# Performance work log

Measured on AMD Instinct MI355X. Metric: run time of the kernel, lower is better.

## Reference

```python
import jax, jax.numpy as jnp
import numpy as np

B = 32           # batch
LATENT = 512     # latent_dim
U = 256          # lstm_units
T = 2048


def setup_inputs() -> dict:
    key = jax.random.key(0)
    ks = jax.random.split(key, 8)
    s = lambda k, shape: jax.random.normal(k, shape, jnp.float32) * 0.05
    return {
        "context_vector": jax.random.normal(ks[0], (B, LATENT), jnp.float32),
        # context_dense: Dense(latent_dim -> lstm_units, relu)
        "Wc": s(ks[1], (LATENT, U)), "bc": jnp.zeros((U,), jnp.float32),
        # lstm1: input dim 2 (coords), keras gate order i,f,g,o in 4*U kernel
        "K1": s(ks[2], (2, 4 * U)), "R1": s(ks[3], (U, 4 * U)), "b1": jnp.zeros((4 * U,), jnp.float32),
        # lstm2: input dim U
        "K2": s(ks[4], (U, 4 * U)), "R2": s(ks[5], (U, 4 * U)), "b2": jnp.zeros((4 * U,), jnp.float32),
        # output_dense: Dense(lstm_units -> 2, sigmoid)
        "Wo": s(ks[6], (U, 2)), "bo": jnp.zeros((2,), jnp.float32),
    }


def _lstm_cell(x, h, c, K, R, b):
    # Keras LSTM cell: gates ordered [i, f, g, o]; sigmoid recurrent activation, tanh activation.
    z = x @ K + h @ R + b                      # [B, 4U]
    i, f, g, o = jnp.split(z, 4, axis=-1)
    c_new = jax.nn.sigmoid(f) * c + jax.nn.sigmoid(i) * jnp.tanh(g)
    h_new = jax.nn.sigmoid(o) * jnp.tanh(c_new)
    return h_new, c_new


def reference(context_vector, Wc, bc, K1, R1, b1, K2, R2, b2, Wo, bo):
    # initial states: h1 = relu(Dense(context)), c1 = h2 = c2 = 0
    h1 = jax.nn.relu(context_vector @ Wc + bc)           # [B, U]
    c1 = jnp.zeros_like(h1)
    h2 = jnp.zeros_like(h1)
    c2 = jnp.zeros_like(h1)
    start = jnp.full((context_vector.shape[0], 2), 0.5, context_vector.dtype)  # start token

    def step(carry, _):
        inp, h1, c1, h2, c2 = carry
        h1, c1 = _lstm_cell(inp, h1, c1, K1, R1, b1)
        h2, c2 = _lstm_cell(h1, h2, c2, K2, R2, b2)
        out = jax.nn.sigmoid(h2 @ Wo + bo)               # [B, 2]
        return (out, h1, c1, h2, c2), out

    _, ys = jax.lax.scan(step, (start, h1, c1, h2, c2), None, length=T)
    return jnp.transpose(ys, (1, 0, 2))                  # [B, T, 2]
```

## Files before the change

### kernel.cpp

```cpp
#include <hip/hip_runtime.h>


#define TSTEPS 2048
#define UNITS  256
#define NB     32
#define NSL    64
#define NTHR   512

typedef float f4 __attribute__((ext_vector_type(4)));

constexpr int CH   = 72;
constexpr int VECF = 4 * CH;
constexpr int BUFW = 4 * VECF;
constexpr int SMEM_BYTES = 84 * 1024;
constexpr int RECF = 8;

__device__ __forceinline__ float sigm(float x) { return 1.f / (1.f + expf(-x)); }

__device__ __forceinline__ float mk_chk(float a, float b, float c, float d, float t) {
  return __fadd_rn(__fadd_rn(__fadd_rn(__fadd_rn(a, b), c), d), t);
}

__device__ __forceinline__ void load_rec(const float* p, f4& a, float& chk) {
  asm volatile("global_load_dwordx4 %0, %2, off sc0 sc1\n\t"
               "global_load_dword %1, %2, off offset:16 sc0 sc1\n\t"
               "s_waitcnt vmcnt(0)"
               : "=&v"(a), "=&v"(chk) : "v"(p) : "memory");
}
__device__ __forceinline__ void store_rec(float* p, const f4& d, float chk) {
  asm volatile("global_store_dwordx4 %0, %1, off sc0 sc1\n\t"
               "global_store_dword %0, %2, off offset:16 sc0 sc1"
               :: "v"(p), "v"(d), "v"(chk) : "memory");
}

__device__ __forceinline__ bool poll2(const float* p0, const float* p1, float tag,
                                      f4& d0, f4& d1, bool ok) {
  if (!ok) return false;
  bool v0 = false, v1 = false;
  int it = 0;
  for (;;) {
    if (!v0) {
      f4 a; float cc; load_rec(p0, a, cc);
      if (__float_as_uint(cc) == __float_as_uint(mk_chk(a.x, a.y, a.z, a.w, tag))) { d0 = a; v0 = true; }
    }
    if (!v1) {
      f4 a; float cc; load_rec(p1, a, cc);
      if (__float_as_uint(cc) == __float_as_uint(mk_chk(a.x, a.y, a.z, a.w, tag))) { d1 = a; v1 = true; }
    }
    if (__all(v0 && v1)) return true;
    if (++it > (1 << 18)) return false;
    if (it > 16) __builtin_amdgcn_s_sleep(1);
  }
}

__device__ __forceinline__ void publish(float* ring, int k, int b, int slice,
                                        int lane, float hn) {
  const float h0 = __shfl(hn, 0), h1 = __shfl(hn, 1),
              h2 = __shfl(hn, 2), h3 = __shfl(hn, 3);
  const float chk = mk_chk(h0, h1, h2, h3, (float)k);
  if (lane == 0) {
    f4 d; d.x = h0; d.y = h1; d.z = h2; d.w = h3;
    store_rec(ring + (((k & 1) * NB + b) * NSL + slice) * RECF, d, chk);
  }
}

__device__ __forceinline__ const float* recp(const float* ring, int k, int b, int sl) {
  return ring + (((k & 1) * NB + b) * NSL + sl) * RECF;
}

__global__ __launch_bounds__(NTHR) void swd_kernel(
    const float* __restrict__ ctx, const float* __restrict__ Wc, const float* __restrict__ bc,
    const float* __restrict__ K1, const float* __restrict__ R1, const float* __restrict__ b1,
    const float* __restrict__ K2, const float* __restrict__ R2, const float* __restrict__ b2,
    const float* __restrict__ Wo, const float* __restrict__ bo,
    float* __restrict__ dout, float* __restrict__ ring1, float* __restrict__ ring2)
{
  extern __shared__ float sm[];
  const int wgid  = blockIdx.x;
  const int layer = wgid >> 7;
  const int half  = (wgid >> 6) & 1;
  const int slice = wgid & 63;
  const int tid = threadIdx.x, lane = tid & 63, wid = tid >> 6;
  const int c = lane & 15, kk = lane >> 4, q = c >> 2, u = c & 3;
  const int gc = q * UNITS + slice * 4 + u;
  const int b0 = half * 16 + wid * 2, b1v = b0 + 1;
  float* buf = sm + wid * BUFW;
  bool ok = true;

  if (layer == 0) {
    float w1[64];
    #pragma unroll
    for (int j = 0; j < 64; ++j) w1[j] = R1[(64 * kk + j) * 1024 + gc];
    const float k1a = K1[gc], k1b = K1[1024 + gc], bb1 = b1[gc];
    float wo0[4], wo1[4];
    #pragma unroll
    for (int m = 0; m < 4; ++m) {
      wo0[m] = Wo[(4 * lane + m) * 2];
      wo1[m] = Wo[(4 * lane + m) * 2 + 1];
    }
    const float bo0 = bo[0], bo1 = bo[1];

    #pragma unroll
    for (int bi = 0; bi < 2; ++bi) {
      const int b = b0 + bi;
      float hv[4];
      #pragma unroll
      for (int uu = 0; uu < 4; ++uu) {
        float p = 0.f;
        const float* cb = ctx + b * 512;
        const float* wc = Wc + slice * 4 + uu;
        #pragma unroll
        for (int m = 0; m < 8; ++m) p = fmaf(cb[lane * 8 + m], wc[(lane * 8 + m) * UNITS], p);
        #pragma unroll
        for (int d = 32; d; d >>= 1) p += __shfl_down(p, d);
        hv[uu] = fmaxf(p + bc[slice * 4 + uu], 0.f);
      }
      const float chk = mk_chk(hv[0], hv[1], hv[2], hv[3], 0.f);
      if (lane == 0) {
        f4 d; d.x = hv[0]; d.y = hv[1]; d.z = hv[2]; d.w = hv[3];
        store_rec(ring1 + ((0 * NB + b) * NSL + slice) * RECF, d, chk);
      }
    }

    float c1a = 0.f, c1b = 0.f;
    float* bufA0 = buf;
    float* bufA1 = buf + VECF;
    for (int s = 0; s < TSTEPS; ++s) {
      f4 d0, d1;
      ok = poll2(recp(ring1, s, b0, lane), recp(ring1, s, b1v, lane), (float)s, d0, d1, ok);
      *(f4*)(bufA0 + kk * CH + 4 * c) = d0;
      *(f4*)(bufA1 + kk * CH + 4 * c) = d1;
      float ax0 = 0.f, ay0 = 0.f, az0 = 0.f, aw0 = 0.f;
      float ax1 = 0.f, ay1 = 0.f, az1 = 0.f, aw1 = 0.f;
      #pragma unroll
      for (int j = 0; j < 16; ++j) {
        const f4 h0 = *(const f4*)(bufA0 + kk * CH + 4 * j);
        const f4 h1 = *(const f4*)(bufA1 + kk * CH + 4 * j);
        ax0 = fmaf(w1[4 * j + 0], h0.x, ax0); ay0 = fmaf(w1[4 * j + 1], h0.y, ay0);
        az0 = fmaf(w1[4 * j + 2], h0.z, az0); aw0 = fmaf(w1[4 * j + 3], h0.w, aw0);
        ax1 = fmaf(w1[4 * j + 0], h1.x, ax1); ay1 = fmaf(w1[4 * j + 1], h1.y, ay1);
        az1 = fmaf(w1[4 * j + 2], h1.z, az1); aw1 = fmaf(w1[4 * j + 3], h1.w, aw1);
      }
      float part0 = (ax0 + ay0) + (az0 + aw0);
      float part1 = (ax1 + ay1) + (az1 + aw1);
      part0 += __shfl_down(part0, 16); part0 += __shfl_down(part0, 32);
      part1 += __shfl_down(part1, 16); part1 += __shfl_down(part1, 32);
      float x00 = 0.5f, x01 = 0.5f, x10 = 0.5f, x11 = 0.5f;
      if (s > 0) {
        f4 g0, g1;
        ok = poll2(recp(ring2, s, b0, lane), recp(ring2, s, b1v, lane), (float)s, g0, g1, ok);
        float po00 = g0.x * wo0[0] + g0.y * wo0[1] + g0.z * wo0[2] + g0.w * wo0[3];
        float po01 = g0.x * wo1[0] + g0.y * wo1[1] + g0.z * wo1[2] + g0.w * wo1[3];
        float po10 = g1.x * wo0[0] + g1.y * wo0[1] + g1.z * wo0[2] + g1.w * wo0[3];
        float po11 = g1.x * wo1[0] + g1.y * wo1[1] + g1.z * wo1[2] + g1.w * wo1[3];
        #pragma unroll
        for (int d = 1; d < 64; d <<= 1) {
          po00 += __shfl_xor(po00, d); po01 += __shfl_xor(po01, d);
          po10 += __shfl_xor(po10, d); po11 += __shfl_xor(po11, d);
        }
        x00 = sigm(po00 + bo0); x01 = sigm(po01 + bo1);
        x10 = sigm(po10 + bo0); x11 = sigm(po11 + bo1);
        if (slice == 0 && lane == 0) {
          *(float2*)(dout + (b0  * TSTEPS + s - 1) * 2) = make_float2(x00, x01);
          *(float2*)(dout + (b1v * TSTEPS + s - 1) * 2) = make_float2(x10, x11);
        }
      }
      {
        const float z = part0 + x00 * k1a + x01 * k1b + bb1;
        const float act = (q == 2) ? tanhf(z) : sigm(z);
        const float gi = __shfl(act, u),     gf = __shfl(act, 4 + u),
                    gg = __shfl(act, 8 + u), go = __shfl(act, 12 + u);
        const float cn = gf * c1a + gi * gg;
        const float hn = go * tanhf(cn);
        c1a = cn;
        publish(ring1, s + 1, b0, slice, lane, hn);
      }
      {
        const float z = part1 + x10 * k1a + x11 * k1b + bb1;
        const float act = (q == 2) ? tanhf(z) : sigm(z);
        const float gi = __shfl(act, u),     gf = __shfl(act, 4 + u),
                    gg = __shfl(act, 8 + u), go = __shfl(act, 12 + u);
        const float cn = gf * c1b + gi * gg;
        const float hn = go * tanhf(cn);
        c1b = cn;
        publish(ring1, s + 1, b1v, slice, lane, hn);
      }
    }
    if (slice == 0) {
      f4 g0, g1;
      ok = poll2(recp(ring2, TSTEPS, b0, lane), recp(ring2, TSTEPS, b1v, lane),
                 (float)TSTEPS, g0, g1, ok);
      float po00 = g0.x * wo0[0] + g0.y * wo0[1] + g0.z * wo0[2] + g0.w * wo0[3];
      float po01 = g0.x * wo1[0] + g0.y * wo1[1] + g0.z * wo1[2] + g0.w * wo1[3];
      float po10 = g1.x * wo0[0] + g1.y * wo0[1] + g1.z * wo0[2] + g1.w * wo0[3];
      float po11 = g1.x * wo1[0] + g1.y * wo1[1] + g1.z * wo1[2] + g1.w * wo1[3];
      #pragma unroll
      for (int d = 1; d < 64; d <<= 1) {
        po00 += __shfl_xor(po00, d); po01 += __shfl_xor(po01, d);
        po10 += __shfl_xor(po10, d); po11 += __shfl_xor(po11, d);
      }
      if (lane == 0) {
        *(float2*)(dout + (b0  * TSTEPS + TSTEPS - 1) * 2) =
            make_float2(sigm(po00 + bo0), sigm(po01 + bo1));
        *(float2*)(dout + (b1v * TSTEPS + TSTEPS - 1) * 2) =
            make_float2(sigm(po10 + bo0), sigm(po11 + bo1));
      }
    }
  } else {
    float wk[64], wr[64];
    #pragma unroll
    for (int j = 0; j < 64; ++j) {
      wk[j] = K2[(64 * kk + j) * 1024 + gc];
      wr[j] = R2[(64 * kk + j) * 1024 + gc];
    }
    const float bb2 = b2[gc];
    float c2a = 0.f, c2b = 0.f;
    float* bh20 = buf;
    float* bh21 = buf + VECF;
    float* bh10 = buf + 2 * VECF;
    float* bh11 = buf + 3 * VECF;
    for (int s = 0; s < TSTEPS; ++s) {
      f4 g0 = {0.f, 0.f, 0.f, 0.f}, g1 = {0.f, 0.f, 0.f, 0.f};
      if (s > 0)
        ok = poll2(recp(ring2, s, b0, lane), recp(ring2, s, b1v, lane), (float)s, g0, g1, ok);
      *(f4*)(bh20 + kk * CH + 4 * c) = g0;
      *(f4*)(bh21 + kk * CH + 4 * c) = g1;
      float rx0 = 0.f, ry0 = 0.f, rz0 = 0.f, rw0 = 0.f;
      float rx1 = 0.f, ry1 = 0.f, rz1 = 0.f, rw1 = 0.f;
      #pragma unroll
      for (int j = 0; j < 16; ++j) {
        const f4 h0 = *(const f4*)(bh20 + kk * CH + 4 * j);
        const f4 h1 = *(const f4*)(bh21 + kk * CH + 4 * j);
        rx0 = fmaf(wr[4 * j + 0], h0.x, rx0); ry0 = fmaf(wr[4 * j + 1], h0.y, ry0);
        rz0 = fmaf(wr[4 * j + 2], h0.z, rz0); rw0 = fmaf(wr[4 * j + 3], h0.w, rw0);
        rx1 = fmaf(wr[4 * j + 0], h1.x, rx1); ry1 = fmaf(wr[4 * j + 1], h1.y, ry1);
        rz1 = fmaf(wr[4 * j + 2], h1.z, rz1); rw1 = fmaf(wr[4 * j + 3], h1.w, rw1);
      }
      f4 d0, d1;
      ok = poll2(recp(ring1, s + 1, b0, lane), recp(ring1, s + 1, b1v, lane),
                 (float)(s + 1), d0, d1, ok);
      *(f4*)(bh10 + kk * CH + 4 * c) = d0;
      *(f4*)(bh11 + kk * CH + 4 * c) = d1;
      float kx0 = 0.f, ky0 = 0.f, kz0 = 0.f, kw0 = 0.f;
      float kx1 = 0.f, ky1 = 0.f, kz1 = 0.f, kw1 = 0.f;
      #pragma unroll
      for (int j = 0; j < 16; ++j) {
        const f4 h0 = *(const f4*)(bh10 + kk * CH + 4 * j);
        const f4 h1 = *(const f4*)(bh11 + kk * CH + 4 * j);
        kx0 = fmaf(wk[4 * j + 0], h0.x, kx0); ky0 = fmaf(wk[4 * j + 1], h0.y, ky0);
        kz0 = fmaf(wk[4 * j + 2], h0.z, kz0); kw0 = fmaf(wk[4 * j + 3], h0.w, kw0);
        kx1 = fmaf(wk[4 * j + 0], h1.x, kx1); ky1 = fmaf(wk[4 * j + 1], h1.y, ky1);
        kz1 = fmaf(wk[4 * j + 2], h1.z, kz1); kw1 = fmaf(wk[4 * j + 3], h1.w, kw1);
      }
      float part0 = ((rx0 + ry0) + (rz0 + rw0)) + ((kx0 + ky0) + (kz0 + kw0));
      float part1 = ((rx1 + ry1) + (rz1 + rw1)) + ((kx1 + ky1) + (kz1 + kw1));
      part0 += __shfl_down(part0, 16); part0 += __shfl_down(part0, 32);
      part1 += __shfl_down(part1, 16); part1 += __shfl_down(part1, 32);
      {
        const float z = part0 + bb2;
        const float act = (q == 2) ? tanhf(z) : sigm(z);
        const float gi = __shfl(act, u),     gf = __shfl(act, 4 + u),
                    gg = __shfl(act, 8 + u), go = __shfl(act, 12 + u);
        const float cn = gf * c2a + gi * gg;
        const float hn = go * tanhf(cn);
        c2a = cn;
        publish(ring2, s + 1, b0, slice, lane, hn);
      }
      {
        const float z = part1 + bb2;
        const float act = (q == 2) ? tanhf(z) : sigm(z);
        const float gi = __shfl(act, u),     gf = __shfl(act, 4 + u),
                    gg = __shfl(act, 8 + u), go = __shfl(act, 12 + u);
        const float cn = gf * c2b + gi * gg;
        const float hn = go * tanhf(cn);
        c2b = cn;
        publish(ring2, s + 1, b1v, slice, lane, hn);
      }
    }
  }
  (void)ok;
}

extern "C" void kernel_launch(void* const* d_in, const int* in_sizes, int n_in,
                              void* d_out, int out_size, void* d_ws, size_t ws_size,
                              hipStream_t stream) {
  (void)in_sizes; (void)n_in; (void)out_size; (void)ws_size;
  const float* ctx = (const float*)d_in[0];
  const float* Wc  = (const float*)d_in[1];
  const float* bc  = (const float*)d_in[2];
  const float* K1  = (const float*)d_in[3];
  const float* R1  = (const float*)d_in[4];
  const float* b1  = (const float*)d_in[5];
  const float* K2  = (const float*)d_in[6];
  const float* R2  = (const float*)d_in[7];
  const float* b2  = (const float*)d_in[8];
  const float* Wo  = (const float*)d_in[9];
  const float* bo  = (const float*)d_in[10];

  float* ring1 = (float*)d_ws;
  float* ring2 = ring1 + 2 * NB * NSL * RECF;

  hipFuncSetAttribute((const void*)swd_kernel,
                      hipFuncAttributeMaxDynamicSharedMemorySize, SMEM_BYTES);
  swd_kernel<<<dim3(256), dim3(NTHR), SMEM_BYTES, stream>>>(
      ctx, Wc, bc, K1, R1, b1, K2, R2, b2, Wo, bo,
      (float*)d_out, ring1, ring2);
}
```

Before: 30.75 ms.

## Issue paired ring polls together, skip self-slice poll, batch output writes

The polling routine now issues both batch-row record loads before one wait instead of two serialized load-wait pairs. Each block keeps its own freshly published slice locally instead of re-reading it from global memory. The poll for the next step moves to the end of the iteration, right after publishing. The writer block buffers sigmoid outputs in shared memory and flushes them as vector stores every 32 steps instead of issuing per-step scalar stores. This shortens the latency of the inter-block handoff on the serial recurrence, at the cost of more restructured control flow and a shorter timeout bound.

```diff
diff --git a/kernel.cpp b/kernel.cpp
--- a/kernel.cpp
+++ b/kernel.cpp
@@ -12,6 +12,7 @@
 constexpr int CH   = 72;
 constexpr int VECF = 4 * CH;
 constexpr int BUFW = 4 * VECF;
+constexpr int HIST_OFF = 8 * BUFW;
 constexpr int SMEM_BYTES = 84 * 1024;
 constexpr int RECF = 8;
 
@@ -21,51 +22,51 @@
   return __fadd_rn(__fadd_rn(__fadd_rn(__fadd_rn(a, b), c), d), t);
 }
 
-__device__ __forceinline__ void load_rec(const float* p, f4& a, float& chk) {
-  asm volatile("global_load_dwordx4 %0, %2, off sc0 sc1\n\t"
-               "global_load_dword %1, %2, off offset:16 sc0 sc1\n\t"
-               "s_waitcnt vmcnt(0)"
-               : "=&v"(a), "=&v"(chk) : "v"(p) : "memory");
-}
 __device__ __forceinline__ void store_rec(float* p, const f4& d, float chk) {
   asm volatile("global_store_dwordx4 %0, %1, off sc0 sc1\n\t"
                "global_store_dword %0, %2, off offset:16 sc0 sc1"
                :: "v"(p), "v"(d), "v"(chk) : "memory");
 }
 
-__device__ __forceinline__ bool poll2(const float* p0, const float* p1, float tag,
-                                      f4& d0, f4& d1, bool ok) {
+__device__ __forceinline__ void load2_rec(const float* p0, const float* p1,
+                                          f4& a0, float& c0, f4& a1, float& c1) {
+  asm volatile("global_load_dwordx4 %0, %4, off sc0 sc1\n\t"
+               "global_load_dword %1, %4, off offset:16 sc0 sc1\n\t"
+               "global_load_dwordx4 %2, %5, off sc0 sc1\n\t"
+               "global_load_dword %3, %5, off offset:16 sc0 sc1\n\t"
+               "s_waitcnt vmcnt(0)"
+               : "=&v"(a0), "=&v"(c0), "=&v"(a1), "=&v"(c1)
+               : "v"(p0), "v"(p1) : "memory");
+}
+
+__device__ __forceinline__ const float* recp(const float* ring, int k, int b, int sl) {
+  return ring + (((k & 1) * NB + b) * NSL + sl) * RECF;
+}
+
+__device__ __forceinline__ bool pollj(const float* p0, const float* p1, float tag,
+                                      f4& d0, f4& d1, bool v0, bool v1, bool ok) {
   if (!ok) return false;
-  bool v0 = false, v1 = false;
   int it = 0;
-  for (;;) {
-    if (!v0) {
-      f4 a; float cc; load_rec(p0, a, cc);
-      if (__float_as_uint(cc) == __float_as_uint(mk_chk(a.x, a.y, a.z, a.w, tag))) { d0 = a; v0 = true; }
-    }
-    if (!v1) {
-      f4 a; float cc; load_rec(p1, a, cc);
-      if (__float_as_uint(cc) == __float_as_uint(mk_chk(a.x, a.y, a.z, a.w, tag))) { d1 = a; v1 = true; }
-    }
-    if (__all(v0 && v1)) return true;
-    if (++it > (1 << 18)) return false;
-    if (it > 16) __builtin_amdgcn_s_sleep(1);
+  while (!__all(v0 && v1)) {
+    f4 a0, a1; float c0, c1;
+    load2_rec(p0, p1, a0, c0, a1, c1);
+    if (!v0 && __float_as_uint(c0) == __float_as_uint(mk_chk(a0.x, a0.y, a0.z, a0.w, tag))) { d0 = a0; v0 = true; }
+    if (!v1 && __float_as_uint(c1) == __float_as_uint(mk_chk(a1.x, a1.y, a1.z, a1.w, tag))) { d1 = a1; v1 = true; }
+    if (++it > (1 << 15)) return false;
+    if (it > 64) __builtin_amdgcn_s_sleep(1);
   }
-}
-
-__device__ __forceinline__ void publish(float* ring, int k, int b, int slice,
-                                        int lane, float hn) {
+  return true;
+}
+
+__device__ __forceinline__ f4 publish(float* ring, int k, int b, int slice,
+                                      int lane, float hn) {
   const float h0 = __shfl(hn, 0), h1 = __shfl(hn, 1),
               h2 = __shfl(hn, 2), h3 = __shfl(hn, 3);
-  const float chk = mk_chk(h0, h1, h2, h3, (float)k);
-  if (lane == 0) {
-    f4 d; d.x = h0; d.y = h1; d.z = h2; d.w = h3;
-    store_rec(ring + (((k & 1) * NB + b) * NSL + slice) * RECF, d, chk);
-  }
-}
-
-__device__ __forceinline__ const float* recp(const float* ring, int k, int b, int sl) {
-  return ring + (((k & 1) * NB + b) * NSL + sl) * RECF;
+  f4 d; d.x = h0; d.y = h1; d.z = h2; d.w = h3;
+  if (lane == 0)
+    store_rec(ring + (((k & 1) * NB + b) * NSL + slice) * RECF, d,
+              mk_chk(h0, h1, h2, h3, (float)k));
+  return d;
 }
 
 __global__ __launch_bounds__(NTHR) void swd_kernel(
@@ -99,11 +100,14 @@
       wo1[m] = Wo[(4 * lane + m) * 2 + 1];
     }
     const float bo0 = bo[0], bo1 = bo[1];
-
+    const bool writer = (slice == 0);
+    float* hist = sm + HIST_OFF + wid * 128;
+
+    f4 self0, self1;
     #pragma unroll
     for (int bi = 0; bi < 2; ++bi) {
       const int b = b0 + bi;
-      float hv[4];
+      float hn = 0.f;
       #pragma unroll
       for (int uu = 0; uu < 4; ++uu) {
         float p = 0.f;
@@ -113,29 +117,29 @@
         for (int m = 0; m < 8; ++m) p = fmaf(cb[lane * 8 + m], wc[(lane * 8 + m) * UNITS], p);
         #pragma unroll
         for (int d = 32; d; d >>= 1) p += __shfl_down(p, d);
-        hv[uu] = fmaxf(p + bc[slice * 4 + uu], 0.f);
-      }
-      const float chk = mk_chk(hv[0], hv[1], hv[2], hv[3], 0.f);
-      if (lane == 0) {
-        f4 d; d.x = hv[0]; d.y = hv[1]; d.z = hv[2]; d.w = hv[3];
-        store_rec(ring1 + ((0 * NB + b) * NSL + slice) * RECF, d, chk);
-      }
+        const float r = __shfl(p, 0);
+        if (lane == uu) hn = fmaxf(r + bc[slice * 4 + uu], 0.f);
+      }
+      const f4 sf = publish(ring1, 0, b, slice, lane, hn);
+      if (bi == 0) self0 = sf; else self1 = sf;
+    }
+    {
+      f4 d0, d1; const bool v = (lane == slice);
+      if (v) { d0 = self0; d1 = self1; }
+      ok = pollj(recp(ring1, 0, b0, lane), recp(ring1, 0, b1v, lane), 0.f, d0, d1, v, v, ok);
+      *(f4*)(buf + kk * CH + 4 * c) = d0;
+      *(f4*)(buf + VECF + kk * CH + 4 * c) = d1;
+      asm volatile("" ::: "memory");
     }
 
     float c1a = 0.f, c1b = 0.f;
-    float* bufA0 = buf;
-    float* bufA1 = buf + VECF;
     for (int s = 0; s < TSTEPS; ++s) {
-      f4 d0, d1;
-      ok = poll2(recp(ring1, s, b0, lane), recp(ring1, s, b1v, lane), (float)s, d0, d1, ok);
-      *(f4*)(bufA0 + kk * CH + 4 * c) = d0;
-      *(f4*)(bufA1 + kk * CH + 4 * c) = d1;
       float ax0 = 0.f, ay0 = 0.f, az0 = 0.f, aw0 = 0.f;
       float ax1 = 0.f, ay1 = 0.f, az1 = 0.f, aw1 = 0.f;
       #pragma unroll
       for (int j = 0; j < 16; ++j) {
-        const f4 h0 = *(const f4*)(bufA0 + kk * CH + 4 * j);
-        const f4 h1 = *(const f4*)(bufA1 + kk * CH + 4 * j);
+        const f4 h0 = *(const f4*)(buf + kk * CH + 4 * j);
+        const f4 h1 = *(const f4*)(buf + VECF + kk * CH + 4 * j);
         ax0 = fmaf(w1[4 * j + 0], h0.x, ax0); ay0 = fmaf(w1[4 * j + 1], h0.y, ay0);
         az0 = fmaf(w1[4 * j + 2], h0.z, az0); aw0 = fmaf(w1[4 * j + 3], h0.w, aw0);
         ax1 = fmaf(w1[4 * j + 0], h1.x, ax1); ay1 = fmaf(w1[4 * j + 1], h1.y, ay1);
@@ -145,10 +149,12 @@
       float part1 = (ax1 + ay1) + (az1 + aw1);
       part0 += __shfl_down(part0, 16); part0 += __shfl_down(part0, 32);
       part1 += __shfl_down(part1, 16); part1 += __shfl_down(part1, 32);
+
       float x00 = 0.5f, x01 = 0.5f, x10 = 0.5f, x11 = 0.5f;
       if (s > 0) {
         f4 g0, g1;
-        ok = poll2(recp(ring2, s, b0, lane), recp(ring2, s, b1v, lane), (float)s, g0, g1, ok);
+        ok = pollj(recp(ring2, s, b0, lane), recp(ring2, s, b1v, lane), (float)s,
+                   g0, g1, false, false, ok);
         float po00 = g0.x * wo0[0] + g0.y * wo0[1] + g0.z * wo0[2] + g0.w * wo0[3];
         float po01 = g0.x * wo1[0] + g0.y * wo1[1] + g0.z * wo1[2] + g0.w * wo1[3];
         float po10 = g1.x * wo0[0] + g1.y * wo0[1] + g1.z * wo0[2] + g1.w * wo0[3];
@@ -160,36 +166,57 @@
         }
         x00 = sigm(po00 + bo0); x01 = sigm(po01 + bo1);
         x10 = sigm(po10 + bo0); x11 = sigm(po11 + bo1);
-        if (slice == 0 && lane == 0) {
-          *(float2*)(dout + (b0  * TSTEPS + s - 1) * 2) = make_float2(x00, x01);
-          *(float2*)(dout + (b1v * TSTEPS + s - 1) * 2) = make_float2(x10, x11);
+        if (writer && lane == 0) {
+          *(float2*)(hist + ((s - 1) & 31) * 2)      = make_float2(x00, x01);
+          *(float2*)(hist + 64 + ((s - 1) & 31) * 2) = make_float2(x10, x11);
         }
       }
-      {
-        const float z = part0 + x00 * k1a + x01 * k1b + bb1;
+
+      {
+        const float z   = part0 + x00 * k1a + x01 * k1b + bb1;
         const float act = (q == 2) ? tanhf(z) : sigm(z);
         const float gi = __shfl(act, u),     gf = __shfl(act, 4 + u),
                     gg = __shfl(act, 8 + u), go = __shfl(act, 12 + u);
         const float cn = gf * c1a + gi * gg;
-        const float hn = go * tanhf(cn);
         c1a = cn;
-        publish(ring1, s + 1, b0, slice, lane, hn);
-      }
-      {
-        const float z = part1 + x10 * k1a + x11 * k1b + bb1;
+        self0 = publish(ring1, s + 1, b0, slice, lane, go * tanhf(cn));
+      }
+      {
+        const float z   = part1 + x10 * k1a + x11 * k1b + bb1;
         const float act = (q == 2) ? tanhf(z) : sigm(z);
         const float gi = __shfl(act, u),     gf = __shfl(act, 4 + u),
                     gg = __shfl(act, 8 + u), go = __shfl(act, 12 + u);
         const float cn = gf * c1b + gi * gg;
-        const float hn = go * tanhf(cn);
         c1b = cn;
-        publish(ring1, s + 1, b1v, slice, lane, hn);
-      }
-    }
-    if (slice == 0) {
+        self1 = publish(ring1, s + 1, b1v, slice, lane, go * tanhf(cn));
+      }
+
+      if (writer && s >= 32 && (s & 31) == 0) {
+        asm volatile("" ::: "memory");
+        if (lane < 16) {
+          const f4 v = *(const f4*)(hist + 4 * lane);
+          *(f4*)(dout + (b0 * TSTEPS + s - 32) * 2 + 4 * lane) = v;
+        } else if (lane < 32) {
+          const f4 v = *(const f4*)(hist + 64 + 4 * (lane - 16));
+          *(f4*)(dout + (b1v * TSTEPS + s - 32) * 2 + 4 * (lane - 16)) = v;
+        }
+      }
+
+      if (s < TSTEPS - 1) {
+        f4 d0, d1; const bool v = (lane == slice);
+        if (v) { d0 = self0; d1 = self1; }
+        ok = pollj(recp(ring1, s + 1, b0, lane), recp(ring1, s + 1, b1v, lane),
+                   (float)(s + 1), d0, d1, v, v, ok);
+        *(f4*)(buf + kk * CH + 4 * c) = d0;
+        *(f4*)(buf + VECF + kk * CH + 4 * c) = d1;
+        asm volatile("" ::: "memory");
+      }
+    }
+
+    if (writer) {
       f4 g0, g1;
-      ok = poll2(recp(ring2, TSTEPS, b0, lane), recp(ring2, TSTEPS, b1v, lane),
-                 (float)TSTEPS, g0, g1, ok);
+      ok = pollj(recp(ring2, TSTEPS, b0, lane), recp(ring2, TSTEPS, b1v, lane),
+                 (float)TSTEPS, g0, g1, false, false, ok);
       float po00 = g0.x * wo0[0] + g0.y * wo0[1] + g0.z * wo0[2] + g0.w * wo0[3];
       float po01 = g0.x * wo1[0] + g0.y * wo1[1] + g0.z * wo1[2] + g0.w * wo1[3];
       float po10 = g1.x * wo0[0] + g1.y * wo0[1] + g1.z * wo0[2] + g1.w * wo0[3];
@@ -200,10 +227,16 @@
         po10 += __shfl_xor(po10, d); po11 += __shfl_xor(po11, d);
       }
       if (lane == 0) {
-        *(float2*)(dout + (b0  * TSTEPS + TSTEPS - 1) * 2) =
-            make_float2(sigm(po00 + bo0), sigm(po01 + bo1));
-        *(float2*)(dout + (b1v * TSTEPS + TSTEPS - 1) * 2) =
-            make_float2(sigm(po10 + bo0), sigm(po11 + bo1));
+        *(float2*)(hist + 31 * 2)      = make_float2(sigm(po00 + bo0), sigm(po01 + bo1));
+        *(float2*)(hist + 64 + 31 * 2) = make_float2(sigm(po10 + bo0), sigm(po11 + bo1));
+      }
+      asm volatile("" ::: "memory");
+      if (lane < 16) {
+        const f4 v = *(const f4*)(hist + 4 * lane);
+        *(f4*)(dout + (b0 * TSTEPS + TSTEPS - 32) * 2 + 4 * lane) = v;
+      } else if (lane < 32) {
+        const f4 v = *(const f4*)(hist + 64 + 4 * (lane - 16));
+        *(f4*)(dout + (b1v * TSTEPS + TSTEPS - 32) * 2 + 4 * (lane - 16)) = v;
       }
     }
   } else {
@@ -219,12 +252,14 @@
     float* bh21 = buf + VECF;
     float* bh10 = buf + 2 * VECF;
     float* bh11 = buf + 3 * VECF;
+    {
+      f4 zz; zz.x = 0.f; zz.y = 0.f; zz.z = 0.f; zz.w = 0.f;
+      *(f4*)(bh20 + kk * CH + 4 * c) = zz;
+      *(f4*)(bh21 + kk * CH + 4 * c) = zz;
+      asm volatile("" ::: "memory");
+    }
+    f4 self0, self1;
     for (int s = 0; s < TSTEPS; ++s) {
-      f4 g0 = {0.f, 0.f, 0.f, 0.f}, g1 = {0.f, 0.f, 0.f, 0.f};
-      if (s > 0)
-        ok = poll2(recp(ring2, s, b0, lane), recp(ring2, s, b1v, lane), (float)s, g0, g1, ok);
-      *(f4*)(bh20 + kk * CH + 4 * c) = g0;
-      *(f4*)(bh21 + kk * CH + 4 * c) = g1;
       float rx0 = 0.f, ry0 = 0.f, rz0 = 0.f, rw0 = 0.f;
       float rx1 = 0.f, ry1 = 0.f, rz1 = 0.f, rw1 = 0.f;
       #pragma unroll
@@ -236,11 +271,14 @@
         rx1 = fmaf(wr[4 * j + 0], h1.x, rx1); ry1 = fmaf(wr[4 * j + 1], h1.y, ry1);
         rz1 = fmaf(wr[4 * j + 2], h1.z, rz1); rw1 = fmaf(wr[4 * j + 3], h1.w, rw1);
       }
-      f4 d0, d1;
-      ok = poll2(recp(ring1, s + 1, b0, lane), recp(ring1, s + 1, b1v, lane),
-                 (float)(s + 1), d0, d1, ok);
-      *(f4*)(bh10 + kk * CH + 4 * c) = d0;
-      *(f4*)(bh11 + kk * CH + 4 * c) = d1;
+      {
+        f4 d0, d1;
+        ok = pollj(recp(ring1, s + 1, b0, lane), recp(ring1, s + 1, b1v, lane),
+                   (float)(s + 1), d0, d1, false, false, ok);
+        *(f4*)(bh10 + kk * CH + 4 * c) = d0;
+        *(f4*)(bh11 + kk * CH + 4 * c) = d1;
+        asm volatile("" ::: "memory");
+      }
       float kx0 = 0.f, ky0 = 0.f, kz0 = 0.f, kw0 = 0.f;
       float kx1 = 0.f, ky1 = 0.f, kz1 = 0.f, kw1 = 0.f;
       #pragma unroll
@@ -257,24 +295,31 @@
       part0 += __shfl_down(part0, 16); part0 += __shfl_down(part0, 32);
       part1 += __shfl_down(part1, 16); part1 += __shfl_down(part1, 32);
       {
-        const float z = part0 + bb2;
+        const float z   = part0 + bb2;
         const float act = (q == 2) ? tanhf(z) : sigm(z);
         const float gi = __shfl(act, u),     gf = __shfl(act, 4 + u),
                     gg = __shfl(act, 8 + u), go = __shfl(act, 12 + u);
         const float cn = gf * c2a + gi * gg;
-        const float hn = go * tanhf(cn);
         c2a = cn;
-        publish(ring2, s + 1, b0, slice, lane, hn);
-      }
-      {
-        const float z = part1 + bb2;
+        self0 = publish(ring2, s + 1, b0, slice, lane, go * tanhf(cn));
+      }
+      {
+        const float z   = part1 + bb2;
         const float act = (q == 2) ? tanhf(z) : sigm(z);
         const float gi = __shfl(act, u),     gf = __shfl(act, 4 + u),
                     gg = __shfl(act, 8 + u), go = __shfl(act, 12 + u);
         const float cn = gf * c2b + gi * gg;
-        const float hn = go * tanhf(cn);
         c2b = cn;
-        publish(ring2, s + 1, b1v, slice, lane, hn);
+        self1 = publish(ring2, s + 1, b1v, slice, lane, go * tanhf(cn));
+      }
+      if (s < TSTEPS - 1) {
+        f4 d0, d1; const bool v = (lane == slice);
+        if (v) { d0 = self0; d1 = self1; }
+        ok = pollj(recp(ring2, s + 1, b0, lane), recp(ring2, s + 1, b1v, lane),
+                   (float)(s + 1), d0, d1, v, v, ok);
+        *(f4*)(bh20 + kk * CH + 4 * c) = d0;
+        *(f4*)(bh21 + kk * CH + 4 * c) = d1;
+        asm volatile("" ::: "memory");
       }
     }
   }
```

Result: slower. 36.38 ms (+18.3%).

## Repartition LSTM across workgroups by batch and unit slice, fusing both layers per block

Applied to the files above, without the earlier changes.

Restructures the persistent kernel so each of 256 workgroups owns one batch row and a 32-unit slice of the gates for both LSTM layers, instead of splitting the layers and batch pairs across separate workgroups. Layer-2 input projection and recurrence are computed in the same block as layer 1, so layer-2 h1 exchange happens through the block's own poll and shared memory. Cross-block exchange now uses one 64-lane poll per ring rather than paired polls. Outputs are buffered in shared memory and written 32 steps at a time. This adds several __syncthreads per step and larger register weight arrays (192 floats per thread), which raises register pressure and risks spills.

```diff
diff --git a/kernel.cpp b/kernel.cpp
--- a/kernel.cpp
+++ b/kernel.cpp
@@ -2,25 +2,17 @@
 
 
 #define TSTEPS 2048
-#define UNITS  256
 #define NB     32
-#define NSL    64
 #define NTHR   512
+#define RECF   8
 
 typedef float f4 __attribute__((ext_vector_type(4)));
-
-constexpr int CH   = 72;
-constexpr int VECF = 4 * CH;
-constexpr int BUFW = 4 * VECF;
-constexpr int SMEM_BYTES = 84 * 1024;
-constexpr int RECF = 8;
 
 __device__ __forceinline__ float sigm(float x) { return 1.f / (1.f + expf(-x)); }
 
 __device__ __forceinline__ float mk_chk(float a, float b, float c, float d, float t) {
   return __fadd_rn(__fadd_rn(__fadd_rn(__fadd_rn(a, b), c), d), t);
 }
-
 __device__ __forceinline__ void load_rec(const float* p, f4& a, float& chk) {
   asm volatile("global_load_dwordx4 %0, %2, off sc0 sc1\n\t"
                "global_load_dword %1, %2, off offset:16 sc0 sc1\n\t"
@@ -32,40 +24,27 @@
                "global_store_dword %0, %2, off offset:16 sc0 sc1"
                :: "v"(p), "v"(d), "v"(chk) : "memory");
 }
-
-__device__ __forceinline__ bool poll2(const float* p0, const float* p1, float tag,
-                                      f4& d0, f4& d1, bool ok) {
+__device__ __forceinline__ float* recp(float* ring, int k, int b, int idx) {
+  return ring + (((k & 1) * NB + b) * 64 + idx) * RECF;
+}
+
+__device__ __forceinline__ bool poll64(const float* ring, int k, int b, float tag,
+                                       int lane, f4& d, bool ok) {
   if (!ok) return false;
-  bool v0 = false, v1 = false;
+  const float* p = ring + (((k & 1) * NB + b) * 64 + lane) * RECF;
+  bool v = false;
   int it = 0;
-  for (;;) {
-    if (!v0) {
-      f4 a; float cc; load_rec(p0, a, cc);
-      if (__float_as_uint(cc) == __float_as_uint(mk_chk(a.x, a.y, a.z, a.w, tag))) { d0 = a; v0 = true; }
-    }
-    if (!v1) {
-      f4 a; float cc; load_rec(p1, a, cc);
-      if (__float_as_uint(cc) == __float_as_uint(mk_chk(a.x, a.y, a.z, a.w, tag))) { d1 = a; v1 = true; }
-    }
-    if (__all(v0 && v1)) return true;
-    if (++it > (1 << 18)) return false;
-    if (it > 16) __builtin_amdgcn_s_sleep(1);
-  }
-}
-
-__device__ __forceinline__ void publish(float* ring, int k, int b, int slice,
-                                        int lane, float hn) {
-  const float h0 = __shfl(hn, 0), h1 = __shfl(hn, 1),
-              h2 = __shfl(hn, 2), h3 = __shfl(hn, 3);
-  const float chk = mk_chk(h0, h1, h2, h3, (float)k);
-  if (lane == 0) {
-    f4 d; d.x = h0; d.y = h1; d.z = h2; d.w = h3;
-    store_rec(ring + (((k & 1) * NB + b) * NSL + slice) * RECF, d, chk);
-  }
-}
-
-__device__ __forceinline__ const float* recp(const float* ring, int k, int b, int sl) {
-  return ring + (((k & 1) * NB + b) * NSL + sl) * RECF;
+  while (!__all(v)) {
+    if (!v) {
+      f4 a; float cc; load_rec(p, a, cc);
+      if (__float_as_uint(cc) == __float_as_uint(mk_chk(a.x, a.y, a.z, a.w, tag))) {
+        d = a; v = true;
+      }
+    }
+    if (++it > (1 << 15)) return false;
+    if (it > 64) __builtin_amdgcn_s_sleep(1);
+  }
+  return true;
 }
 
 __global__ __launch_bounds__(NTHR) void swd_kernel(
@@ -75,207 +54,210 @@
     const float* __restrict__ Wo, const float* __restrict__ bo,
     float* __restrict__ dout, float* __restrict__ ring1, float* __restrict__ ring2)
 {
-  extern __shared__ float sm[];
-  const int wgid  = blockIdx.x;
-  const int layer = wgid >> 7;
-  const int half  = (wgid >> 6) & 1;
-  const int slice = wgid & 63;
-  const int tid = threadIdx.x, lane = tid & 63, wid = tid >> 6;
-  const int c = lane & 15, kk = lane >> 4, q = c >> 2, u = c & 3;
-  const int gc = q * UNITS + slice * 4 + u;
-  const int b0 = half * 16 + wid * 2, b1v = b0 + 1;
-  float* buf = sm + wid * BUFW;
-  bool ok = true;
-
-  if (layer == 0) {
-    float w1[64];
-    #pragma unroll
-    for (int j = 0; j < 64; ++j) w1[j] = R1[(64 * kk + j) * 1024 + gc];
-    const float k1a = K1[gc], k1b = K1[1024 + gc], bb1 = b1[gc];
-    float wo0[4], wo1[4];
+  __shared__ __align__(16) float h1buf[256];
+  __shared__ __align__(16) float h2buf[256];
+  __shared__ float zbuf1[256];
+  __shared__ float zbuf2[1024];
+  __shared__ float gbuf1[128];
+  __shared__ float gbuf2[128];
+  __shared__ float xbuf[2];
+  __shared__ __align__(16) float hist[64];
+
+  const int t    = threadIdx.x;
+  const int wgid = blockIdx.x;
+  const int b    = wgid & 31;
+  const int g    = wgid >> 5;
+  const int lane = t & 63;
+  const bool w0  = (t < 64);
+  const bool w7  = (t >= 448);
+  const int col  = t & 127;
+  const int khq  = t >> 7;
+  const int kh   = khq & 1;
+  const int q    = col >> 5;
+  const int j    = col & 31;
+  const int kcol = q * 256 + 32 * g + j;
+
+  const float* baseA = (t < 256) ? R1 : K2;
+  float wA[128], wB[64];
+  #pragma unroll
+  for (int m = 0; m < 128; ++m) wA[m] = baseA[(kh * 128 + m) * 1024 + kcol];
+  #pragma unroll
+  for (int m = 0; m < 64; ++m) wB[m] = R2[(khq * 64 + m) * 1024 + kcol];
+
+  float k1a = 0.f, k1b = 0.f, bb1 = 0.f, bb2 = 0.f;
+  if (t < 128)      { k1a = K1[kcol]; k1b = K1[1024 + kcol]; bb1 = b1[kcol]; }
+  else if (t < 256) { bb2 = b2[kcol]; }
+  float wo0[4], wo1[4], bo0 = 0.f, bo1 = 0.f;
+  if (w7) {
     #pragma unroll
     for (int m = 0; m < 4; ++m) {
       wo0[m] = Wo[(4 * lane + m) * 2];
       wo1[m] = Wo[(4 * lane + m) * 2 + 1];
     }
-    const float bo0 = bo[0], bo1 = bo[1];
-
-    #pragma unroll
-    for (int bi = 0; bi < 2; ++bi) {
-      const int b = b0 + bi;
-      float hv[4];
-      #pragma unroll
-      for (int uu = 0; uu < 4; ++uu) {
-        float p = 0.f;
-        const float* cb = ctx + b * 512;
-        const float* wc = Wc + slice * 4 + uu;
-        #pragma unroll
-        for (int m = 0; m < 8; ++m) p = fmaf(cb[lane * 8 + m], wc[(lane * 8 + m) * UNITS], p);
-        #pragma unroll
-        for (int d = 32; d; d >>= 1) p += __shfl_down(p, d);
-        hv[uu] = fmaxf(p + bc[slice * 4 + uu], 0.f);
-      }
-      const float chk = mk_chk(hv[0], hv[1], hv[2], hv[3], 0.f);
+    bo0 = bo[0]; bo1 = bo[1];
+  }
+
+  {
+    const int jj = t & 31, kc = t >> 5;
+    float p = 0.f;
+    #pragma unroll
+    for (int m = 0; m < 32; ++m)
+      p = fmaf(ctx[b * 512 + kc * 32 + m], Wc[(kc * 32 + m) * 256 + 32 * g + jj], p);
+    zbuf2[kc * 32 + jj] = p;
+  }
+  if (t == 0) { xbuf[0] = 0.5f; xbuf[1] = 0.5f; }
+  if (t < 256) h2buf[t] = 0.f;
+  __syncthreads();
+
+  bool ok = true;
+  float c1 = 0.f, c2 = 0.f, hn = 0.f;
+  if (t < 32) {
+    float sum = bc[32 * g + t];
+    #pragma unroll
+    for (int kc = 0; kc < 16; ++kc) sum += zbuf2[kc * 32 + t];
+    hn = fmaxf(sum, 0.f);
+  }
+  if (w0) {
+    const float h0  = __shfl(hn, (4 * lane + 0) & 31), h1v = __shfl(hn, (4 * lane + 1) & 31),
+                h2v = __shfl(hn, (4 * lane + 2) & 31), h3v = __shfl(hn, (4 * lane + 3) & 31);
+    if (lane < 8) {
+      f4 dd; dd.x = h0; dd.y = h1v; dd.z = h2v; dd.w = h3v;
+      store_rec(recp(ring1, 0, b, g * 8 + lane), dd, mk_chk(h0, h1v, h2v, h3v, 0.f));
+    }
+  }
+  if (w7) {
+    f4 d;
+    ok = poll64(ring1, 0, b, 0.f, lane, d, ok);
+    *(f4*)(h1buf + 4 * lane) = d;
+  }
+  __syncthreads();
+
+  for (int s = 0; s < TSTEPS; ++s) {
+    if (t < 256) {
+      float a0 = 0.f, a1 = 0.f, a2 = 0.f, a3 = 0.f;
+      const f4* hp = (const f4*)(h1buf + kh * 128);
+      #pragma unroll
+      for (int m = 0; m < 32; ++m) {
+        const f4 hv = hp[m];
+        a0 = fmaf(wA[4 * m + 0], hv.x, a0);
+        a1 = fmaf(wA[4 * m + 1], hv.y, a1);
+        a2 = fmaf(wA[4 * m + 2], hv.z, a2);
+        a3 = fmaf(wA[4 * m + 3], hv.w, a3);
+      }
+      zbuf1[col * 2 + kh] = (a0 + a1) + (a2 + a3);
+    } else if (w7 && s > 0) {
+      f4 gg;
+      ok = poll64(ring2, s, b, (float)s, lane, gg, ok);
+      *(f4*)(h2buf + 4 * lane) = gg;
+      float po0 = gg.x * wo0[0] + gg.y * wo0[1] + gg.z * wo0[2] + gg.w * wo0[3];
+      float po1 = gg.x * wo1[0] + gg.y * wo1[1] + gg.z * wo1[2] + gg.w * wo1[3];
+      #pragma unroll
+      for (int dd = 1; dd < 64; dd <<= 1) { po0 += __shfl_xor(po0, dd); po1 += __shfl_xor(po1, dd); }
+      const float x0 = sigm(po0 + bo0), x1 = sigm(po1 + bo1);
       if (lane == 0) {
-        f4 d; d.x = hv[0]; d.y = hv[1]; d.z = hv[2]; d.w = hv[3];
-        store_rec(ring1 + ((0 * NB + b) * NSL + slice) * RECF, d, chk);
-      }
-    }
-
-    float c1a = 0.f, c1b = 0.f;
-    float* bufA0 = buf;
-    float* bufA1 = buf + VECF;
-    for (int s = 0; s < TSTEPS; ++s) {
-      f4 d0, d1;
-      ok = poll2(recp(ring1, s, b0, lane), recp(ring1, s, b1v, lane), (float)s, d0, d1, ok);
-      *(f4*)(bufA0 + kk * CH + 4 * c) = d0;
-      *(f4*)(bufA1 + kk * CH + 4 * c) = d1;
-      float ax0 = 0.f, ay0 = 0.f, az0 = 0.f, aw0 = 0.f;
-      float ax1 = 0.f, ay1 = 0.f, az1 = 0.f, aw1 = 0.f;
-      #pragma unroll
-      for (int j = 0; j < 16; ++j) {
-        const f4 h0 = *(const f4*)(bufA0 + kk * CH + 4 * j);
-        const f4 h1 = *(const f4*)(bufA1 + kk * CH + 4 * j);
-        ax0 = fmaf(w1[4 * j + 0], h0.x, ax0); ay0 = fmaf(w1[4 * j + 1], h0.y, ay0);
-        az0 = fmaf(w1[4 * j + 2], h0.z, az0); aw0 = fmaf(w1[4 * j + 3], h0.w, aw0);
-        ax1 = fmaf(w1[4 * j + 0], h1.x, ax1); ay1 = fmaf(w1[4 * j + 1], h1.y, ay1);
-        az1 = fmaf(w1[4 * j + 2], h1.z, az1); aw1 = fmaf(w1[4 * j + 3], h1.w, aw1);
-      }
-      float part0 = (ax0 + ay0) + (az0 + aw0);
-      float part1 = (ax1 + ay1) + (az1 + aw1);
-      part0 += __shfl_down(part0, 16); part0 += __shfl_down(part0, 32);
-      part1 += __shfl_down(part1, 16); part1 += __shfl_down(part1, 32);
-      float x00 = 0.5f, x01 = 0.5f, x10 = 0.5f, x11 = 0.5f;
-      if (s > 0) {
-        f4 g0, g1;
-        ok = poll2(recp(ring2, s, b0, lane), recp(ring2, s, b1v, lane), (float)s, g0, g1, ok);
-        float po00 = g0.x * wo0[0] + g0.y * wo0[1] + g0.z * wo0[2] + g0.w * wo0[3];
-        float po01 = g0.x * wo1[0] + g0.y * wo1[1] + g0.z * wo1[2] + g0.w * wo1[3];
-        float po10 = g1.x * wo0[0] + g1.y * wo0[1] + g1.z * wo0[2] + g1.w * wo0[3];
-        float po11 = g1.x * wo1[0] + g1.y * wo1[1] + g1.z * wo1[2] + g1.w * wo1[3];
-        #pragma unroll
-        for (int d = 1; d < 64; d <<= 1) {
-          po00 += __shfl_xor(po00, d); po01 += __shfl_xor(po01, d);
-          po10 += __shfl_xor(po10, d); po11 += __shfl_xor(po11, d);
-        }
-        x00 = sigm(po00 + bo0); x01 = sigm(po01 + bo1);
-        x10 = sigm(po10 + bo0); x11 = sigm(po11 + bo1);
-        if (slice == 0 && lane == 0) {
-          *(float2*)(dout + (b0  * TSTEPS + s - 1) * 2) = make_float2(x00, x01);
-          *(float2*)(dout + (b1v * TSTEPS + s - 1) * 2) = make_float2(x10, x11);
-        }
-      }
-      {
-        const float z = part0 + x00 * k1a + x01 * k1b + bb1;
-        const float act = (q == 2) ? tanhf(z) : sigm(z);
-        const float gi = __shfl(act, u),     gf = __shfl(act, 4 + u),
-                    gg = __shfl(act, 8 + u), go = __shfl(act, 12 + u);
-        const float cn = gf * c1a + gi * gg;
-        const float hn = go * tanhf(cn);
-        c1a = cn;
-        publish(ring1, s + 1, b0, slice, lane, hn);
-      }
-      {
-        const float z = part1 + x10 * k1a + x11 * k1b + bb1;
-        const float act = (q == 2) ? tanhf(z) : sigm(z);
-        const float gi = __shfl(act, u),     gf = __shfl(act, 4 + u),
-                    gg = __shfl(act, 8 + u), go = __shfl(act, 12 + u);
-        const float cn = gf * c1b + gi * gg;
-        const float hn = go * tanhf(cn);
-        c1b = cn;
-        publish(ring1, s + 1, b1v, slice, lane, hn);
-      }
-    }
-    if (slice == 0) {
-      f4 g0, g1;
-      ok = poll2(recp(ring2, TSTEPS, b0, lane), recp(ring2, TSTEPS, b1v, lane),
-                 (float)TSTEPS, g0, g1, ok);
-      float po00 = g0.x * wo0[0] + g0.y * wo0[1] + g0.z * wo0[2] + g0.w * wo0[3];
-      float po01 = g0.x * wo1[0] + g0.y * wo1[1] + g0.z * wo1[2] + g0.w * wo1[3];
-      float po10 = g1.x * wo0[0] + g1.y * wo0[1] + g1.z * wo0[2] + g1.w * wo0[3];
-      float po11 = g1.x * wo1[0] + g1.y * wo1[1] + g1.z * wo1[2] + g1.w * wo1[3];
-      #pragma unroll
-      for (int d = 1; d < 64; d <<= 1) {
-        po00 += __shfl_xor(po00, d); po01 += __shfl_xor(po01, d);
-        po10 += __shfl_xor(po10, d); po11 += __shfl_xor(po11, d);
-      }
-      if (lane == 0) {
-        *(float2*)(dout + (b0  * TSTEPS + TSTEPS - 1) * 2) =
-            make_float2(sigm(po00 + bo0), sigm(po01 + bo1));
-        *(float2*)(dout + (b1v * TSTEPS + TSTEPS - 1) * 2) =
-            make_float2(sigm(po10 + bo0), sigm(po11 + bo1));
-      }
-    }
-  } else {
-    float wk[64], wr[64];
-    #pragma unroll
-    for (int j = 0; j < 64; ++j) {
-      wk[j] = K2[(64 * kk + j) * 1024 + gc];
-      wr[j] = R2[(64 * kk + j) * 1024 + gc];
-    }
-    const float bb2 = b2[gc];
-    float c2a = 0.f, c2b = 0.f;
-    float* bh20 = buf;
-    float* bh21 = buf + VECF;
-    float* bh10 = buf + 2 * VECF;
-    float* bh11 = buf + 3 * VECF;
-    for (int s = 0; s < TSTEPS; ++s) {
-      f4 g0 = {0.f, 0.f, 0.f, 0.f}, g1 = {0.f, 0.f, 0.f, 0.f};
-      if (s > 0)
-        ok = poll2(recp(ring2, s, b0, lane), recp(ring2, s, b1v, lane), (float)s, g0, g1, ok);
-      *(f4*)(bh20 + kk * CH + 4 * c) = g0;
-      *(f4*)(bh21 + kk * CH + 4 * c) = g1;
-      float rx0 = 0.f, ry0 = 0.f, rz0 = 0.f, rw0 = 0.f;
-      float rx1 = 0.f, ry1 = 0.f, rz1 = 0.f, rw1 = 0.f;
-      #pragma unroll
-      for (int j = 0; j < 16; ++j) {
-        const f4 h0 = *(const f4*)(bh20 + kk * CH + 4 * j);
-        const f4 h1 = *(const f4*)(bh21 + kk * CH + 4 * j);
-        rx0 = fmaf(wr[4 * j + 0], h0.x, rx0); ry0 = fmaf(wr[4 * j + 1], h0.y, ry0);
-        rz0 = fmaf(wr[4 * j + 2], h0.z, rz0); rw0 = fmaf(wr[4 * j + 3], h0.w, rw0);
-        rx1 = fmaf(wr[4 * j + 0], h1.x, rx1); ry1 = fmaf(wr[4 * j + 1], h1.y, ry1);
-        rz1 = fmaf(wr[4 * j + 2], h1.z, rz1); rw1 = fmaf(wr[4 * j + 3], h1.w, rw1);
-      }
-      f4 d0, d1;
-      ok = poll2(recp(ring1, s + 1, b0, lane), recp(ring1, s + 1, b1v, lane),
-                 (float)(s + 1), d0, d1, ok);
-      *(f4*)(bh10 + kk * CH + 4 * c) = d0;
-      *(f4*)(bh11 + kk * CH + 4 * c) = d1;
-      float kx0 = 0.f, ky0 = 0.f, kz0 = 0.f, kw0 = 0.f;
-      float kx1 = 0.f, ky1 = 0.f, kz1 = 0.f, kw1 = 0.f;
-      #pragma unroll
-      for (int j = 0; j < 16; ++j) {
-        const f4 h0 = *(const f4*)(bh10 + kk * CH + 4 * j);
-        const f4 h1 = *(const f4*)(bh11 + kk * CH + 4 * j);
-        kx0 = fmaf(wk[4 * j + 0], h0.x, kx0); ky0 = fmaf(wk[4 * j + 1], h0.y, ky0);
-        kz0 = fmaf(wk[4 * j + 2], h0.z, kz0); kw0 = fmaf(wk[4 * j + 3], h0.w, kw0);
-        kx1 = fmaf(wk[4 * j + 0], h1.x, kx1); ky1 = fmaf(wk[4 * j + 1], h1.y, ky1);
-        kz1 = fmaf(wk[4 * j + 2], h1.z, kz1); kw1 = fmaf(wk[4 * j + 3], h1.w, kw1);
-      }
-      float part0 = ((rx0 + ry0) + (rz0 + rw0)) + ((kx0 + ky0) + (kz0 + kw0));
-      float part1 = ((rx1 + ry1) + (rz1 + rw1)) + ((kx1 + ky1) + (kz1 + kw1));
-      part0 += __shfl_down(part0, 16); part0 += __shfl_down(part0, 32);
-      part1 += __shfl_down(part1, 16); part1 += __shfl_down(part1, 32);
-      {
-        const float z = part0 + bb2;
-        const float act = (q == 2) ? tanhf(z) : sigm(z);
-        const float gi = __shfl(act, u),     gf = __shfl(act, 4 + u),
-                    gg = __shfl(act, 8 + u), go = __shfl(act, 12 + u);
-        const float cn = gf * c2a + gi * gg;
-        const float hn = go * tanhf(cn);
-        c2a = cn;
-        publish(ring2, s + 1, b0, slice, lane, hn);
-      }
-      {
-        const float z = part1 + bb2;
-        const float act = (q == 2) ? tanhf(z) : sigm(z);
-        const float gi = __shfl(act, u),     gf = __shfl(act, 4 + u),
-                    gg = __shfl(act, 8 + u), go = __shfl(act, 12 + u);
-        const float cn = gf * c2b + gi * gg;
-        const float hn = go * tanhf(cn);
-        c2b = cn;
-        publish(ring2, s + 1, b1v, slice, lane, hn);
-      }
+        xbuf[0] = x0; xbuf[1] = x1;
+        if (g == 0) { hist[((s - 1) & 31) * 2] = x0; hist[((s - 1) & 31) * 2 + 1] = x1; }
+      }
+    }
+    __syncthreads();
+
+    if (t < 128) {
+      const float z = (zbuf1[2 * t] + zbuf1[2 * t + 1]) + xbuf[0] * k1a + xbuf[1] * k1b + bb1;
+      gbuf1[t] = (q == 2) ? tanhf(z) : sigm(z);
+    }
+    {
+      float a0 = 0.f, a1 = 0.f, a2 = 0.f, a3 = 0.f;
+      const f4* hp = (const f4*)(h2buf + khq * 64);
+      #pragma unroll
+      for (int m = 0; m < 16; ++m) {
+        const f4 hv = hp[m];
+        a0 = fmaf(wB[4 * m + 0], hv.x, a0);
+        a1 = fmaf(wB[4 * m + 1], hv.y, a1);
+        a2 = fmaf(wB[4 * m + 2], hv.z, a2);
+        a3 = fmaf(wB[4 * m + 3], hv.w, a3);
+      }
+      zbuf2[col * 8 + khq] = (a0 + a1) + (a2 + a3);
+    }
+    if (w7 && g == 0 && s >= 32 && (s & 31) == 0 && lane < 16) {
+      const f4 v = *(const f4*)(hist + 4 * lane);
+      *(f4*)(dout + (b * TSTEPS + (s - 32)) * 2 + 4 * lane) = v;
+    }
+    __syncthreads();
+
+    if (t < 32) {
+      const float gi = gbuf1[t], gf = gbuf1[32 + t], gG = gbuf1[64 + t], gO = gbuf1[96 + t];
+      const float cn = gf * c1 + gi * gG;
+      c1 = cn;
+      hn = gO * tanhf(cn);
+    }
+    if (w0) {
+      const float h0  = __shfl(hn, (4 * lane + 0) & 31), h1v = __shfl(hn, (4 * lane + 1) & 31),
+                  h2v = __shfl(hn, (4 * lane + 2) & 31), h3v = __shfl(hn, (4 * lane + 3) & 31);
+      if (lane < 8) {
+        f4 dd; dd.x = h0; dd.y = h1v; dd.z = h2v; dd.w = h3v;
+        store_rec(recp(ring1, s + 1, b, g * 8 + lane), dd,
+                  mk_chk(h0, h1v, h2v, h3v, (float)(s + 1)));
+      }
+    }
+    if (w7) {
+      f4 d;
+      ok = poll64(ring1, s + 1, b, (float)(s + 1), lane, d, ok);
+      *(f4*)(h1buf + 4 * lane) = d;
+    }
+    __syncthreads();
+
+    if (t >= 256) {
+      float a0 = 0.f, a1 = 0.f, a2 = 0.f, a3 = 0.f;
+      const f4* hp = (const f4*)(h1buf + kh * 128);
+      #pragma unroll
+      for (int m = 0; m < 32; ++m) {
+        const f4 hv = hp[m];
+        a0 = fmaf(wA[4 * m + 0], hv.x, a0);
+        a1 = fmaf(wA[4 * m + 1], hv.y, a1);
+        a2 = fmaf(wA[4 * m + 2], hv.z, a2);
+        a3 = fmaf(wA[4 * m + 3], hv.w, a3);
+      }
+      zbuf2[col * 8 + 4 + kh] = (a0 + a1) + (a2 + a3);
+    }
+    __syncthreads();
+
+    if (t >= 128 && t < 256) {
+      const int c = t - 128;
+      const float z = ((zbuf2[c * 8 + 0] + zbuf2[c * 8 + 1]) + (zbuf2[c * 8 + 2] + zbuf2[c * 8 + 3]))
+                    + (zbuf2[c * 8 + 4] + zbuf2[c * 8 + 5]) + bb2;
+      gbuf2[c] = (q == 2) ? tanhf(z) : sigm(z);
+    }
+    __syncthreads();
+
+    if (t >= 32 && t < 64) {
+      const int jj = t - 32;
+      const float gi = gbuf2[jj], gf = gbuf2[32 + jj], gG = gbuf2[64 + jj], gO = gbuf2[96 + jj];
+      const float cn = gf * c2 + gi * gG;
+      c2 = cn;
+      hn = gO * tanhf(cn);
+    }
+    if (w0) {
+      const float h0  = __shfl(hn, 32 + ((4 * lane + 0) & 31)), h1v = __shfl(hn, 32 + ((4 * lane + 1) & 31)),
+                  h2v = __shfl(hn, 32 + ((4 * lane + 2) & 31)), h3v = __shfl(hn, 32 + ((4 * lane + 3) & 31));
+      if (lane >= 32 && lane < 40) {
+        f4 dd; dd.x = h0; dd.y = h1v; dd.z = h2v; dd.w = h3v;
+        store_rec(recp(ring2, s + 1, b, g * 8 + (lane - 32)), dd,
+                  mk_chk(h0, h1v, h2v, h3v, (float)(s + 1)));
+      }
+    }
+  }
+
+  if (g == 0 && w7) {
+    f4 gg;
+    ok = poll64(ring2, TSTEPS, b, (float)TSTEPS, lane, gg, ok);
+    float po0 = gg.x * wo0[0] + gg.y * wo0[1] + gg.z * wo0[2] + gg.w * wo0[3];
+    float po1 = gg.x * wo1[0] + gg.y * wo1[1] + gg.z * wo1[2] + gg.w * wo1[3];
+    #pragma unroll
+    for (int dd = 1; dd < 64; dd <<= 1) { po0 += __shfl_xor(po0, dd); po1 += __shfl_xor(po1, dd); }
+    if (lane == 0) { hist[62] = sigm(po0 + bo0); hist[63] = sigm(po1 + bo1); }
+    if (lane < 16) {
+      const f4 v = *(const f4*)(hist + 4 * lane);
+      *(f4*)(dout + (b * TSTEPS + TSTEPS - 32) * 2 + 4 * lane) = v;
     }
   }
   (void)ok;
@@ -298,11 +280,9 @@
   const float* bo  = (const float*)d_in[10];
 
   float* ring1 = (float*)d_ws;
-  float* ring2 = ring1 + 2 * NB * NSL * RECF;
-
-  hipFuncSetAttribute((const void*)swd_kernel,
-                      hipFuncAttributeMaxDynamicSharedMemorySize, SMEM_BYTES);
-  swd_kernel<<<dim3(256), dim3(NTHR), SMEM_BYTES, stream>>>(
+  float* ring2 = ring1 + 2 * NB * 64 * RECF;
+
+  swd_kernel<<<dim3(256), dim3(NTHR), 0, stream>>>(
       ctx, Wc, bc, K1, R1, b1, K2, R2, b2, Wo, bo,
       (float*)d_out, ring1, ring2);
 }
```

Result: slower. 35.81 ms (+16.5%).
